# Performance work log

Measured on AMD Instinct MI355X. Metric: run time of the kernel, lower is better.

Reference implementation:

```python
import jax, jax.numpy as jnp
import numpy as np

NUM_HEADS = 16

def setup_inputs() -> dict:
    key = jax.random.key(0)
    k1, k2, k3 = jax.random.split(key, 3)
    B, S, D = 4, 2048, 1024
    x = jax.random.normal(k1, (B, S, D), dtype=jnp.float32)
    # xavier-uniform-like small init so unscaled logits stay numerically sane
    w_qkv = jax.random.normal(k2, (3 * D, D), dtype=jnp.float32) * 0.02
    w_out = jax.random.normal(k3, (D, D), dtype=jnp.float32) * 0.02
    return {"x": x, "w_qkv": w_qkv, "w_out": w_out}

def reference(x, w_qkv, w_out):
    B, S, D = x.shape
    H = NUM_HEADS
    d = D // H
    # qkv projection (Linear, no bias): x @ W^T -> [B, S, 3D]
    qkv = jnp.einsum('bsd,ed->bse', x, w_qkv).reshape(B, S, H, 3 * d)
    q, k, v = jnp.split(qkv, 3, axis=-1)           # each [B, S, H, d]
    q = q.transpose(0, 2, 1, 3)                    # [B, H, S, d]
    k = k.transpose(0, 2, 1, 3)
    v = v.transpose(0, 2, 1, 3)
    # NOTE: the original module does NOT scale by 1/sqrt(d) — faithful.
    logits = jnp.einsum('bhqd,bhkd->bhqk', q, k)   # [B, H, S, S]
    attn = jax.nn.softmax(logits, axis=-1)
    vals = jnp.einsum('bhqk,bhkd->bhqd', attn, v)  # [B, H, S, d]
    vals = vals.transpose(0, 2, 1, 3).reshape(B, S, D)
    return jnp.einsum('bsd,od->bso', vals, w_out)
```

## Files before the change

kernel.cpp:

```cpp
#include <hip/hip_runtime.h>
#include <hip/hip_bf16.h>

#define DEVINL __device__ __forceinline__

typedef short bf16x4 __attribute__((ext_vector_type(4)));
typedef short bf16x8 __attribute__((ext_vector_type(8)));
typedef float f32x4 __attribute__((ext_vector_type(4)));
typedef float f32x16 __attribute__((ext_vector_type(16)));
typedef unsigned short us4 __attribute__((ext_vector_type(4)));


DEVINL unsigned short f2bf(float f) {
  unsigned u = __builtin_bit_cast(unsigned, f);
  unsigned r = u + 0x7fffu + ((u >> 16) & 1u);
  return (unsigned short)(r >> 16);
}

DEVINL f32x4 mfma32(bf16x8 a, bf16x8 b, f32x4 c) {
  return __builtin_amdgcn_mfma_f32_16x16x32_bf16(a, b, c, 0, 0, 0);
}

DEVINL f32x16 mfma3216(bf16x8 a, bf16x8 b, f32x16 c) {
  return __builtin_amdgcn_mfma_f32_32x32x16_bf16(a, b, c, 0, 0, 0);
}

DEVINL unsigned cvt_pk_bf16(float a, float b) {
  unsigned r;
  asm("v_cvt_pk_bf16_f32 %0, %1, %2" : "=v"(r) : "v"(a), "v"(b));
  return r;
}

DEVINL void permswap(unsigned& x, unsigned& y) {
#if __has_builtin(__builtin_amdgcn_permlane32_swap)
  typedef int i32x2_t __attribute__((ext_vector_type(2)));
  i32x2_t r = __builtin_amdgcn_permlane32_swap((int)x, (int)y, false, false);
  x = (unsigned)r[0];
  y = (unsigned)r[1];
#else
  asm("v_permlane32_swap_b32 %0, %1" : "+v"(x), "+v"(y));
#endif
}

#define GLOAD_LDS16(g, l)                                                    \
  __builtin_amdgcn_global_load_lds(                                          \
      (__attribute__((address_space(1))) void*)(unsigned short*)(g),         \
      (__attribute__((address_space(3))) void*)(l), 16, 0, 0)

__global__ void cvtk(const float* __restrict__ src,
                     unsigned short* __restrict__ dst, int n4) {
  int i = blockIdx.x * 256 + threadIdx.x;
  const int st = gridDim.x * 256;
  for (; i < n4; i += st) {
    const float4 v = ((const float4*)src)[i];
    us4 o;
    o[0] = f2bf(v.x); o[1] = f2bf(v.y); o[2] = f2bf(v.z); o[3] = f2bf(v.w);
    ((us4*)dst)[i] = o;
  }
}

__global__ __launch_bounds__(256, 2) void qkv_gemm(
    const unsigned short* __restrict__ A,
    const unsigned short* __restrict__ Bw,
    unsigned short* __restrict__ Qo,
    unsigned short* __restrict__ Ko,
    unsigned short* __restrict__ VTo) {
  constexpr int K = 1024, BK = 32;
  __shared__ unsigned short As[128 * BK];
  __shared__ unsigned short Bs[128 * BK];
  const int tid = threadIdx.x;
  const int lane = tid & 63;
  const int wid = tid >> 6;
  const int l15 = lane & 15, g = lane >> 4;
  const int fid = blockIdx.y * 24 + blockIdx.x;
  const int swzid = (fid & 7) * 192 + (fid >> 3);
  const int m0 = (swzid / 24) * 128;
  const int n0 = (swzid % 24) * 128;
  const int wr = wid >> 1, wc = wid & 1;

  f32x4 acc[4][4] = {};

  const int sidx0 = tid * 8;
  const int sidx1 = (256 + tid) * 8;
  const int r0 = sidx0 >> 5, c0 = sidx0 & 31;
  const int r1 = sidx1 >> 5, c1 = sidx1 & 31;

  for (int k0 = 0; k0 < K; k0 += BK) {
    __syncthreads();
    GLOAD_LDS16(A + (size_t)(m0 + r0) * K + k0 + c0, As + sidx0);
    GLOAD_LDS16(Bw + (size_t)(n0 + r0) * K + k0 + c0, Bs + sidx0);
    GLOAD_LDS16(A + (size_t)(m0 + r1) * K + k0 + c1, As + sidx1);
    GLOAD_LDS16(Bw + (size_t)(n0 + r1) * K + k0 + c1, Bs + sidx1);
    __syncthreads();
    bf16x8 af[4], bfr[4];
#pragma unroll
    for (int i = 0; i < 4; ++i) {
      af[i] = *(const bf16x8*)(As + (wr * 64 + i * 16 + l15) * BK + g * 8);
      bfr[i] = *(const bf16x8*)(Bs + (wc * 64 + i * 16 + l15) * BK + g * 8);
    }
#pragma unroll
    for (int mi = 0; mi < 4; ++mi)
#pragma unroll
      for (int ni = 0; ni < 4; ++ni)
        acc[mi][ni] = mfma32(af[mi], bfr[ni], acc[mi][ni]);
  }

#pragma unroll
  for (int mi = 0; mi < 4; ++mi) {
    const int mbase = m0 + wr * 64 + mi * 16 + g * 4;
#pragma unroll
    for (int ni = 0; ni < 4; ++ni) {
      const int e = n0 + wc * 64 + ni * 16 + l15;
      const int h = e / 192;
      const int r = e - h * 192;
#pragma unroll
      for (int j = 0; j < 4; ++j) {
        const int mm = mbase + j;
        const int b = mm >> 11, s = mm & 2047;
        const int bh = b * 16 + h;
        if (r < 64)
          Qo[((size_t)bh * 2048 + s) * 64 + r] =
              f2bf(acc[mi][ni][j] * 1.44269504f);
        else if (r < 128)
          Ko[((size_t)bh * 2048 + s) * 64 + (r - 64)] = f2bf(acc[mi][ni][j]);
        else
          VTo[((size_t)bh * 64 + (r - 128)) * 2048 + s] = f2bf(acc[mi][ni][j]);
      }
    }
  }
}

__global__ __launch_bounds__(256, 2) void attn_fwd(
    const unsigned short* __restrict__ Q,
    const unsigned short* __restrict__ K,
    const unsigned short* __restrict__ VT,
    unsigned short* __restrict__ Vals) {
  __shared__ unsigned short Ks[2][64 * 64];
  __shared__ unsigned short Vs[2][64 * 64];
  __shared__ float invs[4][2][32];
  const int tid = threadIdx.x;
  const int lane = tid & 63;
  const int wid = tid >> 6;
  const int l31 = lane & 31;
  const int hi = lane >> 5;
  const int bid = (blockIdx.x & 7) * 64 + (blockIdx.x >> 3);
  const int bh = bid >> 3;
  const int q0 = (bid & 7) * 256 + wid * 64;
  const unsigned short* Qb = Q + (size_t)bh * (2048 * 64);
  const unsigned short* Kb = K + (size_t)bh * (2048 * 64);
  const unsigned short* Vb = VT + (size_t)bh * (64 * 2048);

  const int i0 = tid, i1 = tid + 256;
  const int sr0 = i0 >> 3, sr1 = i1 >> 3;
  const int sc0 = ((((i0 & 7) << 4) ^ ((sr0 & 7) << 4)) >> 1);
  const int sc1 = ((((i1 & 7) << 4) ^ ((sr1 & 7) << 4)) >> 1);

#define STAGE(kv0, nb)                                                      \
  {                                                                         \
    GLOAD_LDS16(Kb + (size_t)((kv0) + sr0) * 64 + sc0, &Ks[nb][i0 * 8]);    \
    GLOAD_LDS16(Kb + (size_t)((kv0) + sr1) * 64 + sc1, &Ks[nb][i1 * 8]);    \
    GLOAD_LDS16(Vb + (size_t)sr0 * 2048 + (kv0) + sc0, &Vs[nb][i0 * 8]);    \
    GLOAD_LDS16(Vb + (size_t)sr1 * 2048 + (kv0) + sc1, &Vs[nb][i1 * 8]);    \
  }

  bf16x8 qf[2][4];
#pragma unroll
  for (int qt = 0; qt < 2; ++qt) {
    const unsigned short* qrow = Qb + (size_t)(q0 + qt * 32 + l31) * 64;
#pragma unroll
    for (int kw = 0; kw < 4; ++kw)
      qf[qt][kw] = *(const bf16x8*)(qrow + kw * 16 + hi * 8);
  }

  float lsum[2] = {0.0f, 0.0f};
  f32x16 o[2][2] = {};
  const int swz = (l31 & 7) << 4;

  STAGE(0, 0);
  __syncthreads();

  for (int kv0 = 0; kv0 < 2048; kv0 += 64) {
    const int cur = (kv0 >> 6) & 1;
    if (kv0 + 64 < 2048) STAGE(kv0 + 64, cur ^ 1);
    const char* kb = (const char*)Ks[cur];
    const char* vb = (const char*)Vs[cur];
#pragma unroll
    for (int sub = 0; sub < 2; ++sub) {
      bf16x8 kf[4];
#pragma unroll
      for (int kw = 0; kw < 4; ++kw)
        kf[kw] = *(const bf16x8*)(kb + (sub * 32 + l31) * 128 +
                                  ((kw * 32 + hi * 16) ^ swz));
      f32x16 s[2];
      __builtin_amdgcn_s_setprio(1);
#pragma unroll
      for (int qt = 0; qt < 2; ++qt) {
        f32x16 t = {};
#pragma unroll
        for (int kw = 0; kw < 4; ++kw) t = mfma3216(kf[kw], qf[qt][kw], t);
        s[qt] = t;
      }
      __builtin_amdgcn_s_setprio(0);
      float p[2][16];
#pragma unroll
      for (int qt = 0; qt < 2; ++qt) {
#pragma unroll
        for (int j = 0; j < 16; ++j) p[qt][j] = exp2f(s[qt][j]);
        lsum[qt] += ((((p[qt][0] + p[qt][1]) + (p[qt][2] + p[qt][3])) +
                      ((p[qt][4] + p[qt][5]) + (p[qt][6] + p[qt][7]))) +
                     (((p[qt][8] + p[qt][9]) + (p[qt][10] + p[qt][11])) +
                      ((p[qt][12] + p[qt][13]) + (p[qt][14] + p[qt][15]))));
      }
#pragma unroll
      for (int half = 0; half < 2; ++half) {
        const int pb = half * 8;
        bf16x8 pa[2];
#pragma unroll
        for (int qt = 0; qt < 2; ++qt) {
          unsigned w0 = cvt_pk_bf16(p[qt][pb + 0], p[qt][pb + 1]);
          unsigned w2 = cvt_pk_bf16(p[qt][pb + 4], p[qt][pb + 5]);
          permswap(w0, w2);
          unsigned w1 = cvt_pk_bf16(p[qt][pb + 2], p[qt][pb + 3]);
          unsigned w3 = cvt_pk_bf16(p[qt][pb + 6], p[qt][pb + 7]);
          permswap(w1, w3);
          union {
            unsigned u[4];
            bf16x8 v;
          } pk;
          pk.u[0] = w0;
          pk.u[1] = w1;
          pk.u[2] = w2;
          pk.u[3] = w3;
          pa[qt] = pk.v;
        }
        const int ksoff = (sub * 2 + half) * 32;
        const bf16x8 vf0 =
            *(const bf16x8*)(vb + l31 * 128 + ((ksoff + hi * 16) ^ swz));
        const bf16x8 vf1 = *(const bf16x8*)(vb + (32 + l31) * 128 +
                                            ((ksoff + hi * 16) ^ swz));
        __builtin_amdgcn_s_setprio(1);
        o[0][0] = mfma3216(pa[0], vf0, o[0][0]);
        o[0][1] = mfma3216(pa[0], vf1, o[0][1]);
        o[1][0] = mfma3216(pa[1], vf0, o[1][0]);
        o[1][1] = mfma3216(pa[1], vf1, o[1][1]);
        __builtin_amdgcn_s_setprio(0);
      }
    }
    __syncthreads();
  }
#undef STAGE

#pragma unroll
  for (int qt = 0; qt < 2; ++qt) {
    const float ltot = lsum[qt] + __shfl_xor(lsum[qt], 32);
    invs[wid][qt][l31] = 1.0f / ltot;
  }
  const int b = bh >> 4, h = bh & 15;
#pragma unroll
  for (int qt = 0; qt < 2; ++qt) {
    unsigned short* ob =
        Vals + (size_t)(b * 2048 + q0 + qt * 32) * 1024 + h * 64 + l31;
#pragma unroll
    for (int j = 0; j < 16; ++j) {
      const int ql = (j & 3) + 8 * (j >> 2) + 4 * hi;
      const float inv = invs[wid][qt][ql];
      ob[(size_t)ql * 1024] = f2bf(o[qt][0][j] * inv);
      ob[(size_t)ql * 1024 + 32] = f2bf(o[qt][1][j] * inv);
    }
  }
}

__global__ __launch_bounds__(256, 2) void out_gemm(
    const unsigned short* __restrict__ A,
    const unsigned short* __restrict__ Bw,
    float* __restrict__ C) {
  constexpr int K = 1024, BK = 32;
  __shared__ unsigned short As[128 * BK];
  __shared__ unsigned short Bs[128 * BK];
  const int tid = threadIdx.x;
  const int lane = tid & 63;
  const int wid = tid >> 6;
  const int l15 = lane & 15, g = lane >> 4;
  const int fid = blockIdx.y * 8 + blockIdx.x;
  const int swzid = (fid & 7) * 64 + (fid >> 3);
  const int m0 = (swzid >> 3) * 128;
  const int n0 = (swzid & 7) * 128;
  const int wr = wid >> 1, wc = wid & 1;

  f32x4 acc[4][4] = {};

  const int sidx0 = tid * 8;
  const int sidx1 = (256 + tid) * 8;
  const int r0 = sidx0 >> 5, c0 = sidx0 & 31;
  const int r1 = sidx1 >> 5, c1 = sidx1 & 31;

  for (int k0 = 0; k0 < K; k0 += BK) {
    __syncthreads();
    GLOAD_LDS16(A + (size_t)(m0 + r0) * K + k0 + c0, As + sidx0);
    GLOAD_LDS16(Bw + (size_t)(n0 + r0) * K + k0 + c0, Bs + sidx0);
    GLOAD_LDS16(A + (size_t)(m0 + r1) * K + k0 + c1, As + sidx1);
    GLOAD_LDS16(Bw + (size_t)(n0 + r1) * K + k0 + c1, Bs + sidx1);
    __syncthreads();
    bf16x8 af[4], bfr[4];
#pragma unroll
    for (int i = 0; i < 4; ++i) {
      af[i] = *(const bf16x8*)(As + (wr * 64 + i * 16 + l15) * BK + g * 8);
      bfr[i] = *(const bf16x8*)(Bs + (wc * 64 + i * 16 + l15) * BK + g * 8);
    }
#pragma unroll
    for (int mi = 0; mi < 4; ++mi)
#pragma unroll
      for (int ni = 0; ni < 4; ++ni)
        acc[mi][ni] = mfma32(af[mi], bfr[ni], acc[mi][ni]);
  }

#pragma unroll
  for (int mi = 0; mi < 4; ++mi) {
    const int mbase = m0 + wr * 64 + mi * 16 + g * 4;
#pragma unroll
    for (int ni = 0; ni < 4; ++ni) {
      const int n = n0 + wc * 64 + ni * 16 + l15;
#pragma unroll
      for (int j = 0; j < 4; ++j)
        C[(size_t)(mbase + j) * 1024 + n] = acc[mi][ni][j];
    }
  }
}

extern "C" void kernel_launch(void* const* d_in, const int* in_sizes, int n_in,
                              void* d_out, int out_size, void* d_ws,
                              size_t ws_size, hipStream_t stream) {
  const float* x = (const float*)d_in[0];
  const float* w_qkv = (const float*)d_in[1];
  const float* w_out = (const float*)d_in[2];
  float* out = (float*)d_out;

  char* ws = (char*)d_ws;
  unsigned short* xb = (unsigned short*)(ws);
  unsigned short* wqkvb = (unsigned short*)(ws + (16u << 20));
  unsigned short* woutb = (unsigned short*)(ws + (22u << 20));
  unsigned short* Qt = (unsigned short*)(ws + (24u << 20));
  unsigned short* Kt = (unsigned short*)(ws + (40u << 20));
  unsigned short* VTt = (unsigned short*)(ws + (56u << 20));
  unsigned short* vals = xb;

  cvtk<<<2048, 256, 0, stream>>>(x, xb, 8388608 / 4);
  cvtk<<<2048, 256, 0, stream>>>(w_qkv, wqkvb, 3145728 / 4);
  cvtk<<<1024, 256, 0, stream>>>(w_out, woutb, 1048576 / 4);
  qkv_gemm<<<dim3(24, 64), 256, 0, stream>>>(xb, wqkvb, Qt, Kt, VTt);
  attn_fwd<<<512, 256, 0, stream>>>(Qt, Kt, VTt, vals);
  out_gemm<<<dim3(8, 64), 256, 0, stream>>>(vals, woutb, out);
}
```

Measured before the change: 223.5 us.

## Double KV tile to 128 keys, use raw v_exp_f32, precompute swizzled LDS offsets

The attention kernel now stages 128 keys of K and V^T per iteration instead of 64, which halves the number of loop iterations and block barriers and issues more async global-to-LDS loads per stage. exp2f is replaced by an inline v_exp_f32, which drops the library's range and denormal handling. LDS read addresses are precomputed per lane and combined with XOR offsets to cut address arithmetic. LDS use per block doubles to about 64KB, which may limit occupancy with two blocks per CU.

Measured after the change: 211.6 us. 5.3% less time.

```diff
diff --git a/kernel.cpp b/kernel.cpp
--- a/kernel.cpp
+++ b/kernel.cpp
@@ -22,6 +22,12 @@
 
 DEVINL f32x16 mfma3216(bf16x8 a, bf16x8 b, f32x16 c) {
   return __builtin_amdgcn_mfma_f32_32x32x16_bf16(a, b, c, 0, 0, 0);
+}
+
+DEVINL float fexp2(float x) {
+  float r;
+  asm("v_exp_f32 %0, %1" : "=v"(r) : "v"(x));
+  return r;
 }
 
 DEVINL unsigned cvt_pk_bf16(float a, float b) {
@@ -134,8 +140,8 @@
     const unsigned short* __restrict__ K,
     const unsigned short* __restrict__ VT,
     unsigned short* __restrict__ Vals) {
-  __shared__ unsigned short Ks[2][64 * 64];
-  __shared__ unsigned short Vs[2][64 * 64];
+  __shared__ unsigned short Ks[2][128 * 64];
+  __shared__ unsigned short Vs[2][64 * 128];
   __shared__ float invs[4][2][32];
   const int tid = threadIdx.x;
   const int lane = tid & 63;
@@ -149,19 +155,6 @@
   const unsigned short* Kb = K + (size_t)bh * (2048 * 64);
   const unsigned short* Vb = VT + (size_t)bh * (64 * 2048);
 
-  const int i0 = tid, i1 = tid + 256;
-  const int sr0 = i0 >> 3, sr1 = i1 >> 3;
-  const int sc0 = ((((i0 & 7) << 4) ^ ((sr0 & 7) << 4)) >> 1);
-  const int sc1 = ((((i1 & 7) << 4) ^ ((sr1 & 7) << 4)) >> 1);
-
-#define STAGE(kv0, nb)                                                      \
-  {                                                                         \
-    GLOAD_LDS16(Kb + (size_t)((kv0) + sr0) * 64 + sc0, &Ks[nb][i0 * 8]);    \
-    GLOAD_LDS16(Kb + (size_t)((kv0) + sr1) * 64 + sc1, &Ks[nb][i1 * 8]);    \
-    GLOAD_LDS16(Vb + (size_t)sr0 * 2048 + (kv0) + sc0, &Vs[nb][i0 * 8]);    \
-    GLOAD_LDS16(Vb + (size_t)sr1 * 2048 + (kv0) + sc1, &Vs[nb][i1 * 8]);    \
-  }
-
   bf16x8 qf[2][4];
 #pragma unroll
   for (int qt = 0; qt < 2; ++qt) {
@@ -173,23 +166,38 @@
 
   float lsum[2] = {0.0f, 0.0f};
   f32x16 o[2][2] = {};
-  const int swz = (l31 & 7) << 4;
+  const unsigned swz = (unsigned)((l31 & 7) << 4);
+  const unsigned laneK = (unsigned)(l31 * 128) + (((unsigned)hi << 4) ^ swz);
+  const unsigned laneV = (unsigned)(l31 * 256) + (((unsigned)hi << 4) ^ swz);
+
+#define STAGE(kv0, nb)                                                       \
+  {                                                                          \
+    _Pragma("unroll") for (int j = 0; j < 4; ++j) {                          \
+      const int c = tid + j * 256;                                           \
+      const int kr = c >> 3;                                                 \
+      const int ksc = ((((c & 7) << 4) ^ ((kr & 7) << 4)) >> 1);             \
+      GLOAD_LDS16(Kb + (size_t)((kv0) + kr) * 64 + ksc, &Ks[nb][c * 8]);     \
+      const int vr = c >> 4;                                                 \
+      const int vsc = ((((c & 15) << 4) ^ ((vr & 7) << 4)) >> 1);            \
+      GLOAD_LDS16(Vb + (size_t)vr * 2048 + (kv0) + vsc, &Vs[nb][c * 8]);     \
+    }                                                                        \
+  }
 
   STAGE(0, 0);
   __syncthreads();
 
-  for (int kv0 = 0; kv0 < 2048; kv0 += 64) {
-    const int cur = (kv0 >> 6) & 1;
-    if (kv0 + 64 < 2048) STAGE(kv0 + 64, cur ^ 1);
+  for (int kv0 = 0; kv0 < 2048; kv0 += 128) {
+    const int cur = (kv0 >> 7) & 1;
+    if (kv0 + 128 < 2048) STAGE(kv0 + 128, cur ^ 1);
     const char* kb = (const char*)Ks[cur];
     const char* vb = (const char*)Vs[cur];
 #pragma unroll
-    for (int sub = 0; sub < 2; ++sub) {
+    for (int sub = 0; sub < 4; ++sub) {
+      const unsigned kbase = laneK + (unsigned)(sub * 4096);
       bf16x8 kf[4];
 #pragma unroll
       for (int kw = 0; kw < 4; ++kw)
-        kf[kw] = *(const bf16x8*)(kb + (sub * 32 + l31) * 128 +
-                                  ((kw * 32 + hi * 16) ^ swz));
+        kf[kw] = *(const bf16x8*)(kb + (kbase ^ (unsigned)(kw * 32)));
       f32x16 s[2];
       __builtin_amdgcn_s_setprio(1);
 #pragma unroll
@@ -204,7 +212,7 @@
 #pragma unroll
       for (int qt = 0; qt < 2; ++qt) {
 #pragma unroll
-        for (int j = 0; j < 16; ++j) p[qt][j] = exp2f(s[qt][j]);
+        for (int j = 0; j < 16; ++j) p[qt][j] = fexp2(s[qt][j]);
         lsum[qt] += ((((p[qt][0] + p[qt][1]) + (p[qt][2] + p[qt][3])) +
                       ((p[qt][4] + p[qt][5]) + (p[qt][6] + p[qt][7]))) +
                      (((p[qt][8] + p[qt][9]) + (p[qt][10] + p[qt][11])) +
@@ -232,11 +240,9 @@
           pk.u[3] = w3;
           pa[qt] = pk.v;
         }
-        const int ksoff = (sub * 2 + half) * 32;
-        const bf16x8 vf0 =
-            *(const bf16x8*)(vb + l31 * 128 + ((ksoff + hi * 16) ^ swz));
-        const bf16x8 vf1 = *(const bf16x8*)(vb + (32 + l31) * 128 +
-                                            ((ksoff + hi * 16) ^ swz));
+        const unsigned ksoff = (unsigned)((sub * 2 + half) * 32);
+        const bf16x8 vf0 = *(const bf16x8*)(vb + (laneV ^ ksoff));
+        const bf16x8 vf1 = *(const bf16x8*)(vb + ((laneV + 8192u) ^ ksoff));
         __builtin_amdgcn_s_setprio(1);
         o[0][0] = mfma3216(pa[0], vf0, o[0][0]);
         o[0][1] = mfma3216(pa[0], vf1, o[0][1]);
```
